# Kernel tuning notes

Hardware: AMD Instinct MI355X
Metric: run time of the kernel (lower is better)

## Reference

```python
import jax, jax.numpy as jnp
import numpy as np

LEAKY_ALPHA = 0.2  # TF default for tf.nn.leaky_relu


def setup_inputs() -> dict:
    key = jax.random.key(0)
    ks = jax.random.split(key, 5)
    B, N, F, O, H = 2, 4096, 256, 64, 4
    x = jax.random.normal(ks[0], (B, N, F), dtype=jnp.float32)
    bias = jax.random.normal(ks[1], (B, N, N), dtype=jnp.float32)
    W = jax.random.normal(ks[2], (H, F, O), dtype=jnp.float32) * (1.0 / np.sqrt(F))
    a = jax.random.normal(ks[3], (H, O), dtype=jnp.float32) * (1.0 / np.sqrt(O))
    b = jax.random.normal(ks[4], (H, O), dtype=jnp.float32) * 0.01
    return {"x": x, "bias": bias, "W": W, "a": a, "b": b}


def reference(x, bias, W, a, b):
    # x: [B,N,F], bias: [B,N,N], W: [H,F,O], a: [H,O], b: [H,O]
    h = jnp.einsum('bnf,hfo->bhno', x, W)          # transformed inputs per head
    w = jnp.einsum('bhno,ho->bhn', h, a)           # scalar score per node
    scores = w[:, :, :, None] + w[:, :, None, :]   # [B,H,N,N]: w_i + w_j
    logits = jax.nn.leaky_relu(scores, LEAKY_ALPHA) + bias[:, None, :, :]
    coefs = jax.nn.softmax(logits, axis=3)
    heads = jnp.einsum('bhnm,bhmo->bhno', coefs, h) + b[None, :, None, :]
    return jnp.mean(heads, axis=1)                 # (1/H) * sum of heads -> [B,N,O]
```

## Files before the change

### kernel.cpp

```cpp
#include <hip/hip_runtime.h>
#include <hip/hip_bf16.h>


constexpr int Bc = 2, Nc = 4096, Fc = 256, Oc = 64, Hc = 4;
constexpr float ALPHA = 0.2f;
constexpr float LOG2E = 1.4426950408889634f;

typedef __attribute__((ext_vector_type(8))) short bf16x8;
typedef __attribute__((ext_vector_type(4))) float f32x4;

static __device__ inline short f2bf(float x) {
    __hip_bfloat16 h = __float2bfloat16(x);
    return *reinterpret_cast<short*>(&h);
}

static __device__ inline int frag_off(int jt, int k, int lane, int t) {
    return jt * 4096 + k * 512 + lane * 8 + t;
}

__global__ __launch_bounds__(256) void k_h(const float* __restrict__ x,
                                           const float* __restrict__ W,
                                           const float* __restrict__ a,
                                           short* __restrict__ hTB,
                                           float* __restrict__ wout) {
    __shared__ float xs[64][132];
    const int nb = Nc / 64;
    const int blk = blockIdx.x;
    const int nt = blk % nb;
    const int bh = blk / nb;
    const int h = bh % Hc;
    const int b = bh / Hc;
    const int tid = threadIdx.x;
    const int o_id = tid & 15, n_id = tid >> 4;
    const int o0 = o_id * 4, n0 = n_id * 4;

    float acc[4][4] = {};

    for (int fs = 0; fs < Fc; fs += 128) {
#pragma unroll
        for (int it = 0; it < 8; ++it) {
            int idx = it * 256 + tid;
            int r = idx >> 5, c = idx & 31;
            const float4 v = *reinterpret_cast<const float4*>(
                &x[((size_t)(b * Nc + nt * 64 + r)) * Fc + fs + c * 4]);
            *reinterpret_cast<float4*>(&xs[r][c * 4]) = v;
        }
        __syncthreads();
        for (int f = 0; f < 128; ++f) {
            const float4 wv = *reinterpret_cast<const float4*>(
                &W[((size_t)(h * Fc + fs + f)) * Oc + o0]);
            float xv[4];
#pragma unroll
            for (int r = 0; r < 4; ++r) xv[r] = xs[n0 + r][f];
#pragma unroll
            for (int r = 0; r < 4; ++r) {
                acc[r][0] = __builtin_fmaf(xv[r], wv.x, acc[r][0]);
                acc[r][1] = __builtin_fmaf(xv[r], wv.y, acc[r][1]);
                acc[r][2] = __builtin_fmaf(xv[r], wv.z, acc[r][2]);
                acc[r][3] = __builtin_fmaf(xv[r], wv.w, acc[r][3]);
            }
        }
        __syncthreads();
    }

    const float4 av = *reinterpret_cast<const float4*>(&a[h * Oc + o0]);
    float part[4];
#pragma unroll
    for (int r = 0; r < 4; ++r) {
        part[r] = acc[r][0] * av.x + acc[r][1] * av.y + acc[r][2] * av.z +
                  acc[r][3] * av.w;
#pragma unroll
        for (int off = 1; off < 16; off <<= 1)
            part[r] += __shfl_xor(part[r], off, 64);
    }
    const int n_glob = nt * 64 + n0;
    if (o_id == 0) {
#pragma unroll
        for (int r = 0; r < 4; ++r)
            wout[((size_t)(b * Hc + h)) * Nc + n_glob + r] = part[r];
    }
    const int sub = n0 >> 5;
    const int lg = (n0 >> 3) & 3;
    const int t0 = n0 & 7;
    short* base = hTB + ((size_t)(b * Hc + h)) * (Nc * Oc);
#pragma unroll
    for (int c = 0; c < 4; ++c) {
        const int o = o0 + c;
        const int of = o >> 4, li = o & 15;
        short4 v;
        v.x = f2bf(acc[0][c]);
        v.y = f2bf(acc[1][c]);
        v.z = f2bf(acc[2][c]);
        v.w = f2bf(acc[3][c]);
        *reinterpret_cast<short4*>(&base[frag_off(nt, of * 2 + sub, lg * 16 + li, t0)]) = v;
    }
}

__global__ __launch_bounds__(1024, 4) void k_attn(
    const float* __restrict__ bias, const float* __restrict__ bvec,
    const float* __restrict__ wrow, const short* __restrict__ hTB,
    float* __restrict__ out) {
    __shared__ float accs[16][16][64];
    __shared__ float ml[16][2][16];
    float* bias_sm = &accs[0][0][0];

    const int blk = blockIdx.x;
    const int b = blk / (Nc / 16);
    const int i0 = (blk % (Nc / 16)) * 16;
    const int tid = threadIdx.x;
    const int w = tid >> 6;
    const int hd = w & 3;
    const int c4 = w >> 2;
    const int lane = tid & 63;
    const int li = lane & 15, lg = lane >> 4;
    const int jl0 = lg * 8;

    const float wi = wrow[((size_t)(b * Hc + hd)) * Nc + i0 + li];
    const float* __restrict__ wj_base = &wrow[((size_t)(b * Hc + hd)) * Nc];
    const short* __restrict__ fb =
        hTB + ((size_t)(b * Hc + hd)) * (Nc * Oc) + lane * 8;

    const int scol = tid & 63;
    const float* __restrict__ stage_src =
        &bias[((size_t)(b * Nc + i0 + w)) * Nc + scol];
    float* stage_dst = bias_sm + w * 257 + scol;

    f32x4 acc[4] = {{0.f, 0.f, 0.f, 0.f},
                    {0.f, 0.f, 0.f, 0.f},
                    {0.f, 0.f, 0.f, 0.f},
                    {0.f, 0.f, 0.f, 0.f}};
    float m_run = -1e30f, l_run = 0.f;

    float pre[4];
#pragma unroll
    for (int k2 = 0; k2 < 4; ++k2) pre[k2] = stage_src[64 * k2];
#pragma unroll
    for (int k2 = 0; k2 < 4; ++k2) stage_dst[64 * k2] = pre[k2];
    __syncthreads();

    int buf = 0;
#pragma unroll 1
    for (int st = 0; st < 16; ++st) {
        if (st < 15) {
#pragma unroll
            for (int k2 = 0; k2 < 4; ++k2)
                pre[k2] = stage_src[(size_t)(st + 1) * 256 + 64 * k2];
        }
        const int jt = st * 4 + c4;
        bf16x8 fr[8];
#pragma unroll
        for (int k = 0; k < 8; ++k)
            fr[k] = *reinterpret_cast<const bf16x8*>(fb + jt * 4096 + k * 512);
        const float* bsm = bias_sm + buf * 4112 + li * 257 + c4 * 64 + jl0;
        float s[16];
#pragma unroll
        for (int t = 0; t < 8; ++t) {
            s[t] = bsm[t];
            s[8 + t] = bsm[32 + t];
        }
        const int j0 = st * 256 + c4 * 64;
#pragma unroll
        for (int u = 0; u < 4; ++u) {
            const float4 wv = *reinterpret_cast<const float4*>(
                &wj_base[j0 + (u >> 1) * 32 + jl0 + (u & 1) * 4]);
            float v;
            v = wi + wv.x; s[u * 4 + 0] += fmaxf(v, ALPHA * v);
            v = wi + wv.y; s[u * 4 + 1] += fmaxf(v, ALPHA * v);
            v = wi + wv.z; s[u * 4 + 2] += fmaxf(v, ALPHA * v);
            v = wi + wv.w; s[u * 4 + 3] += fmaxf(v, ALPHA * v);
        }
        float mx = s[0];
#pragma unroll
        for (int t = 1; t < 16; ++t) mx = fmaxf(mx, s[t]);
        mx = fmaxf(mx, __shfl_xor(mx, 16, 64));
        mx = fmaxf(mx, __shfl_xor(mx, 32, 64));
        const float m_new = fmaxf(m_run, mx);
        const float scale = __builtin_amdgcn_exp2f((m_run - m_new) * LOG2E);
        const float mL = m_new * LOG2E;
        float tsum = 0.f;
#pragma unroll
        for (int t = 0; t < 16; ++t) {
            s[t] = __builtin_amdgcn_exp2f(__builtin_fmaf(s[t], LOG2E, -mL));
            tsum += s[t];
        }
        tsum += __shfl_xor(tsum, 16, 64);
        tsum += __shfl_xor(tsum, 32, 64);
        l_run = l_run * scale + tsum;
        m_run = m_new;
        float sc[4];
#pragma unroll
        for (int r = 0; r < 4; ++r) sc[r] = __shfl(scale, lg * 4 + r, 64);
#pragma unroll
        for (int of = 0; of < 4; ++of) {
            acc[of][0] *= sc[0];
            acc[of][1] *= sc[1];
            acc[of][2] *= sc[2];
            acc[of][3] *= sc[3];
        }
        bf16x8 pa[2];
#pragma unroll
        for (int sub = 0; sub < 2; ++sub)
#pragma unroll
            for (int t = 0; t < 8; ++t) pa[sub][t] = f2bf(s[sub * 8 + t]);
        __builtin_amdgcn_s_setprio(1);
#pragma unroll
        for (int of = 0; of < 4; ++of) {
            acc[of] = __builtin_amdgcn_mfma_f32_16x16x32_bf16(pa[0], fr[of * 2 + 0],
                                                              acc[of], 0, 0, 0);
            acc[of] = __builtin_amdgcn_mfma_f32_16x16x32_bf16(pa[1], fr[of * 2 + 1],
                                                              acc[of], 0, 0, 0);
        }
        __builtin_amdgcn_s_setprio(0);
        if (st < 15) {
#pragma unroll
            for (int k2 = 0; k2 < 4; ++k2)
                stage_dst[(buf ^ 1) * 4112 + 64 * k2] = pre[k2];
        }
        __syncthreads();
        buf ^= 1;
    }

#pragma unroll
    for (int of = 0; of < 4; ++of)
#pragma unroll
        for (int r = 0; r < 4; ++r)
            accs[w][lg * 4 + r][of * 16 + li] = acc[of][r];
    if (lg == 0) {
        ml[w][0][li] = m_run;
        ml[w][1][li] = l_run;
    }
    __syncthreads();

    const int row = tid >> 6, col = tid & 63;
    float osum = 0.f;
#pragma unroll
    for (int h = 0; h < 4; ++h) {
        float mq[4], lq[4];
#pragma unroll
        for (int qq = 0; qq < 4; ++qq) {
            mq[qq] = ml[qq * 4 + h][0][row];
            lq[qq] = ml[qq * 4 + h][1][row];
        }
        const float M = fmaxf(fmaxf(mq[0], mq[1]), fmaxf(mq[2], mq[3]));
        float l = 0.f, A = 0.f;
#pragma unroll
        for (int qq = 0; qq < 4; ++qq) {
            const float f = __builtin_amdgcn_exp2f((mq[qq] - M) * LOG2E);
            l = __builtin_fmaf(f, lq[qq], l);
            A = __builtin_fmaf(f, accs[qq * 4 + h][row][col], A);
        }
        osum += A / l;
    }
    const float bm = 0.25f * (bvec[col] + bvec[Oc + col] + bvec[2 * Oc + col] +
                              bvec[3 * Oc + col]);
    out[((size_t)(b * Nc + i0 + row)) * Oc + col] = 0.25f * osum + bm;
}

extern "C" void kernel_launch(void* const* d_in, const int* in_sizes, int n_in,
                              void* d_out, int out_size, void* d_ws, size_t ws_size,
                              hipStream_t stream) {
    const float* x = (const float*)d_in[0];
    const float* bias = (const float*)d_in[1];
    const float* W = (const float*)d_in[2];
    const float* a = (const float*)d_in[3];
    const float* bvec = (const float*)d_in[4];
    float* out = (float*)d_out;

    short* hTB = (short*)d_ws;
    float* wbuf = (float*)((char*)d_ws + (size_t)Bc * Hc * Oc * Nc * 2);

    k_h<<<Bc * Hc * (Nc / 64), 256, 0, stream>>>(x, W, a, hTB, wbuf);
    k_attn<<<Bc * (Nc / 16), 1024, 0, stream>>>(bias, bvec, wbuf, hTB, out);
}
```

Measured before the change: 106.5 us.

## Halve attention block size, defer online-softmax rescale, vectorize bias staging

```diff
diff --git a/kernel.cpp b/kernel.cpp
--- a/kernel.cpp
+++ b/kernel.cpp
@@ -5,6 +5,7 @@
 constexpr int Bc = 2, Nc = 4096, Fc = 256, Oc = 64, Hc = 4;
 constexpr float ALPHA = 0.2f;
 constexpr float LOG2E = 1.4426950408889634f;
+constexpr float DEFER_THR = 8.0f;
 
 typedef __attribute__((ext_vector_type(8))) short bf16x8;
 typedef __attribute__((ext_vector_type(4))) float f32x4;
@@ -96,13 +97,13 @@
     }
 }
 
-__global__ __launch_bounds__(1024, 4) void k_attn(
+__global__ __launch_bounds__(512, 5) void k_attn(
     const float* __restrict__ bias, const float* __restrict__ bvec,
     const float* __restrict__ wrow, const short* __restrict__ hTB,
     float* __restrict__ out) {
-    __shared__ float accs[16][16][64];
-    __shared__ float ml[16][2][16];
-    float* bias_sm = &accs[0][0][0];
+    __shared__ float accs[8][16][64];
+    __shared__ float bsm[2][16][132];
+    __shared__ float ml[8][2][16];
 
     const int blk = blockIdx.x;
     const int b = blk / (Nc / 16);
@@ -110,7 +111,7 @@
     const int tid = threadIdx.x;
     const int w = tid >> 6;
     const int hd = w & 3;
-    const int c4 = w >> 2;
+    const int c2 = w >> 2;
     const int lane = tid & 63;
     const int li = lane & 15, lg = lane >> 4;
     const int jl0 = lg * 8;
@@ -120,45 +121,40 @@
     const short* __restrict__ fb =
         hTB + ((size_t)(b * Hc + hd)) * (Nc * Oc) + lane * 8;
 
-    const int scol = tid & 63;
+    const int srow = tid >> 5, scol4 = tid & 31;
     const float* __restrict__ stage_src =
-        &bias[((size_t)(b * Nc + i0 + w)) * Nc + scol];
-    float* stage_dst = bias_sm + w * 257 + scol;
+        &bias[((size_t)(b * Nc + i0 + srow)) * Nc + scol4 * 4];
 
     f32x4 acc[4] = {{0.f, 0.f, 0.f, 0.f},
                     {0.f, 0.f, 0.f, 0.f},
                     {0.f, 0.f, 0.f, 0.f},
                     {0.f, 0.f, 0.f, 0.f}};
-    float m_run = -1e30f, l_run = 0.f;
-
-    float pre[4];
-#pragma unroll
-    for (int k2 = 0; k2 < 4; ++k2) pre[k2] = stage_src[64 * k2];
-#pragma unroll
-    for (int k2 = 0; k2 < 4; ++k2) stage_dst[64 * k2] = pre[k2];
+    float m_run = -1e30f;
+    float l_run = 0.f;
+
+    float4 pre = *reinterpret_cast<const float4*>(stage_src);
+    *reinterpret_cast<float4*>(&bsm[0][srow][scol4 * 4]) = pre;
     __syncthreads();
 
     int buf = 0;
 #pragma unroll 1
-    for (int st = 0; st < 16; ++st) {
-        if (st < 15) {
-#pragma unroll
-            for (int k2 = 0; k2 < 4; ++k2)
-                pre[k2] = stage_src[(size_t)(st + 1) * 256 + 64 * k2];
-        }
-        const int jt = st * 4 + c4;
+    for (int st = 0; st < 32; ++st) {
+        if (st < 31)
+            pre = *reinterpret_cast<const float4*>(stage_src + (size_t)(st + 1) * 128);
+
+        const int jt = st * 2 + c2;
+        const int j0 = jt * 64;
         bf16x8 fr[8];
 #pragma unroll
         for (int k = 0; k < 8; ++k)
             fr[k] = *reinterpret_cast<const bf16x8*>(fb + jt * 4096 + k * 512);
-        const float* bsm = bias_sm + buf * 4112 + li * 257 + c4 * 64 + jl0;
-        float s[16];
-#pragma unroll
-        for (int t = 0; t < 8; ++t) {
-            s[t] = bsm[t];
-            s[8 + t] = bsm[32 + t];
-        }
-        const int j0 = st * 256 + c4 * 64;
+        const float* bp = &bsm[buf][li][c2 * 64 + jl0];
+        const float4 b03 = *reinterpret_cast<const float4*>(bp);
+        const float4 b47 = *reinterpret_cast<const float4*>(bp + 4);
+        const float4 b8b = *reinterpret_cast<const float4*>(bp + 32);
+        const float4 bcf = *reinterpret_cast<const float4*>(bp + 36);
+        float s[16] = {b03.x, b03.y, b03.z, b03.w, b47.x, b47.y, b47.z, b47.w,
+                       b8b.x, b8b.y, b8b.z, b8b.w, bcf.x, bcf.y, bcf.z, bcf.w};
 #pragma unroll
         for (int u = 0; u < 4; ++u) {
             const float4 wv = *reinterpret_cast<const float4*>(
@@ -169,34 +165,38 @@
             v = wi + wv.z; s[u * 4 + 2] += fmaxf(v, ALPHA * v);
             v = wi + wv.w; s[u * 4 + 3] += fmaxf(v, ALPHA * v);
         }
-        float mx = s[0];
-#pragma unroll
-        for (int t = 1; t < 16; ++t) mx = fmaxf(mx, s[t]);
-        mx = fmaxf(mx, __shfl_xor(mx, 16, 64));
-        mx = fmaxf(mx, __shfl_xor(mx, 32, 64));
-        const float m_new = fmaxf(m_run, mx);
-        const float scale = __builtin_amdgcn_exp2f((m_run - m_new) * LOG2E);
-        const float mL = m_new * LOG2E;
+        float m01 = fmaxf(s[0], s[1]), m23 = fmaxf(s[2], s[3]);
+        float m45 = fmaxf(s[4], s[5]), m67 = fmaxf(s[6], s[7]);
+        float m89 = fmaxf(s[8], s[9]), mab = fmaxf(s[10], s[11]);
+        float mcd = fmaxf(s[12], s[13]), mef = fmaxf(s[14], s[15]);
+        float mx = fmaxf(fmaxf(fmaxf(m01, m23), fmaxf(m45, m67)),
+                         fmaxf(fmaxf(m89, mab), fmaxf(mcd, mef)));
+        if (!__all(mx <= m_run + DEFER_THR)) {
+            float rmx = fmaxf(mx, __shfl_xor(mx, 16, 64));
+            rmx = fmaxf(rmx, __shfl_xor(rmx, 32, 64));
+            const float m_new = fmaxf(m_run, rmx);
+            const float scale = __builtin_amdgcn_exp2f((m_run - m_new) * LOG2E);
+            l_run *= scale;
+            float sc[4];
+#pragma unroll
+            for (int r = 0; r < 4; ++r) sc[r] = __shfl(scale, lg * 4 + r, 64);
+#pragma unroll
+            for (int of = 0; of < 4; ++of) {
+                acc[of][0] *= sc[0];
+                acc[of][1] *= sc[1];
+                acc[of][2] *= sc[2];
+                acc[of][3] *= sc[3];
+            }
+            m_run = m_new;
+        }
+        const float mL = m_run * LOG2E;
         float tsum = 0.f;
 #pragma unroll
         for (int t = 0; t < 16; ++t) {
             s[t] = __builtin_amdgcn_exp2f(__builtin_fmaf(s[t], LOG2E, -mL));
             tsum += s[t];
         }
-        tsum += __shfl_xor(tsum, 16, 64);
-        tsum += __shfl_xor(tsum, 32, 64);
-        l_run = l_run * scale + tsum;
-        m_run = m_new;
-        float sc[4];
-#pragma unroll
-        for (int r = 0; r < 4; ++r) sc[r] = __shfl(scale, lg * 4 + r, 64);
-#pragma unroll
-        for (int of = 0; of < 4; ++of) {
-            acc[of][0] *= sc[0];
-            acc[of][1] *= sc[1];
-            acc[of][2] *= sc[2];
-            acc[of][3] *= sc[3];
-        }
+        l_run += tsum;
         bf16x8 pa[2];
 #pragma unroll
         for (int sub = 0; sub < 2; ++sub)
@@ -211,15 +211,14 @@
                                                               acc[of], 0, 0, 0);
         }
         __builtin_amdgcn_s_setprio(0);
-        if (st < 15) {
-#pragma unroll
-            for (int k2 = 0; k2 < 4; ++k2)
-                stage_dst[(buf ^ 1) * 4112 + 64 * k2] = pre[k2];
-        }
+        if (st < 31)
+            *reinterpret_cast<float4*>(&bsm[buf ^ 1][srow][scol4 * 4]) = pre;
         __syncthreads();
         buf ^= 1;
     }
 
+    float l_row = l_run + __shfl_xor(l_run, 16, 64);
+    l_row += __shfl_xor(l_row, 32, 64);
 #pragma unroll
     for (int of = 0; of < 4; ++of)
 #pragma unroll
@@ -227,33 +226,31 @@
             accs[w][lg * 4 + r][of * 16 + li] = acc[of][r];
     if (lg == 0) {
         ml[w][0][li] = m_run;
-        ml[w][1][li] = l_run;
+        ml[w][1][li] = l_row;
     }
     __syncthreads();
 
-    const int row = tid >> 6, col = tid & 63;
-    float osum = 0.f;
-#pragma unroll
-    for (int h = 0; h < 4; ++h) {
-        float mq[4], lq[4];
-#pragma unroll
-        for (int qq = 0; qq < 4; ++qq) {
-            mq[qq] = ml[qq * 4 + h][0][row];
-            lq[qq] = ml[qq * 4 + h][1][row];
-        }
-        const float M = fmaxf(fmaxf(mq[0], mq[1]), fmaxf(mq[2], mq[3]));
-        float l = 0.f, A = 0.f;
-#pragma unroll
-        for (int qq = 0; qq < 4; ++qq) {
-            const float f = __builtin_amdgcn_exp2f((mq[qq] - M) * LOG2E);
-            l = __builtin_fmaf(f, lq[qq], l);
-            A = __builtin_fmaf(f, accs[qq * 4 + h][row][col], A);
-        }
-        osum += A / l;
-    }
-    const float bm = 0.25f * (bvec[col] + bvec[Oc + col] + bvec[2 * Oc + col] +
-                              bvec[3 * Oc + col]);
-    out[((size_t)(b * Nc + i0 + row)) * Oc + col] = 0.25f * osum + bm;
+#pragma unroll
+    for (int k = 0; k < 2; ++k) {
+        const int e = k * 512 + tid;
+        const int row = e >> 6, col = e & 63;
+        float osum = 0.f;
+#pragma unroll
+        for (int h = 0; h < 4; ++h) {
+            const float m0 = ml[h][0][row], m1 = ml[4 + h][0][row];
+            const float l0 = ml[h][1][row], l1 = ml[4 + h][1][row];
+            const float M = fmaxf(m0, m1);
+            const float f0 = __builtin_amdgcn_exp2f((m0 - M) * LOG2E);
+            const float f1 = __builtin_amdgcn_exp2f((m1 - M) * LOG2E);
+            const float l = f0 * l0 + f1 * l1;
+            const float A =
+                f0 * accs[h][row][col] + f1 * accs[4 + h][row][col];
+            osum += A / l;
+        }
+        const float bm = 0.25f * (bvec[col] + bvec[Oc + col] + bvec[2 * Oc + col] +
+                                  bvec[3 * Oc + col]);
+        out[((size_t)(b * Nc + i0 + row)) * Oc + col] = 0.25f * osum + bm;
+    }
 }
 
 extern "C" void kernel_launch(void* const* d_in, const int* in_sizes, int n_in,
@@ -270,5 +267,5 @@
     float* wbuf = (float*)((char*)d_ws + (size_t)Bc * Hc * Oc * Nc * 2);
 
     k_h<<<Bc * Hc * (Nc / 64), 256, 0, stream>>>(x, W, a, hTB, wbuf);
-    k_attn<<<Bc * (Nc / 16), 1024, 0, stream>>>(bias, bvec, wbuf, hTB, out);
-}
+    k_attn<<<Bc * (Nc / 16), 512, 0, stream>>>(bias, bvec, wbuf, hTB, out);
+}
```

New measurement: 115.7 us. +8.7%, slower.
